# Kernel tuning notes

Hardware: AMD Instinct MI355X
Metric: run time of the kernel (lower is better)

Reference implementation:

```python
import jax, jax.numpy as jnp
import numpy as np

B, H, W, C = 16, 64, 64, 384
DH = 32                 # dim_head
NH = C // DH            # heads = dim // dim_head
WS = 8                  # window_size
DFF = 4 * C             # dim_ff default = 4*dim
EPS = 1e-5


def setup_inputs() -> dict:
    key = jax.random.key(0)
    ks = jax.random.split(key, 6)
    rn = lambda k, shape, scale: (jax.random.normal(k, shape, jnp.float32) * scale)
    return {
        "x": rn(ks[0], (B, H, W, C), 1.0),
        "w_qkv": rn(ks[1], (C, 3 * NH * DH), 0.02),   # fused qkv projection, bias=False
        "w_out": rn(ks[2], (NH * DH, C), 0.02),       # attention output projection
        "gamma_attn": jnp.ones((C,), jnp.float32),     # LayerNormNoBias2d weight (post-attn)
        "w1": rn(ks[3], (C, DFF), 0.02),               # FFN up projection
        "w2": rn(ks[4], (DFF, C), 0.02),               # FFN down projection
        "gamma_ff": jnp.ones((C,), jnp.float32),       # LayerNormNoBias2d weight (post-FFN)
    }


def _shift2d(x):
    # S2-MLP style 4-way spatial shift of channel quarters, zero-filled at borders.
    c4 = x.shape[-1] // 4
    g1 = jnp.pad(x[:, :-1, :, 0 * c4:1 * c4], ((0, 0), (1, 0), (0, 0), (0, 0)))  # shift down
    g2 = jnp.pad(x[:, 1:, :, 1 * c4:2 * c4], ((0, 0), (0, 1), (0, 0), (0, 0)))   # shift up
    g3 = jnp.pad(x[:, :, :-1, 2 * c4:3 * c4], ((0, 0), (0, 0), (1, 0), (0, 0)))  # shift right
    g4 = jnp.pad(x[:, :, 1:, 3 * c4:4 * c4], ((0, 0), (0, 0), (0, 1), (0, 0)))   # shift left
    return jnp.concatenate([g1, g2, g3, g4], axis=-1)


def _ln_nobias(x, gamma):
    # LayerNorm over channel dim, weight only (no bias).
    mu = jnp.mean(x, axis=-1, keepdims=True)
    var = jnp.var(x, axis=-1, keepdims=True)
    return (x - mu) * jax.lax.rsqrt(var + EPS) * gamma


def _window_attention(x, w_qkv, w_out):
    # Grouped (non-overlapping) window multi-head self-attention.
    b, h, w, c = x.shape
    nh, nw = h // WS, w // WS
    T = WS * WS
    # partition into windows: (b*nh*nw, T, c)
    xw = x.reshape(b, nh, WS, nw, WS, c).transpose(0, 1, 3, 2, 4, 5).reshape(b * nh * nw, T, c)
    qkv = xw @ w_qkv                                   # (n, T, 3*NH*DH)
    qkv = qkv.reshape(-1, T, 3, NH, DH)
    q = qkv[:, :, 0].transpose(0, 2, 1, 3)             # (n, NH, T, DH)
    k = qkv[:, :, 1].transpose(0, 2, 1, 3)
    v = qkv[:, :, 2].transpose(0, 2, 1, 3)
    logits = jnp.einsum('nhqd,nhkd->nhqk', q, k) * (DH ** -0.5)
    attn = jax.nn.softmax(logits, axis=-1)
    o = jnp.einsum('nhqk,nhkd->nhqd', attn, v)         # (n, NH, T, DH)
    o = o.transpose(0, 2, 1, 3).reshape(-1, T, NH * DH) @ w_out
    # un-window back to (b, h, w, c)
    return o.reshape(b, nh, nw, WS, WS, c).transpose(0, 1, 3, 2, 4, 5).reshape(b, h, w, c)


def reference(x, w_qkv, w_out, gamma_attn, w1, w2, gamma_ff):
    # x = x + DropBlock(Norm(GWAttn(Shift2d(x))))   (drop rates = 0 -> identity)
    a = _window_attention(_shift2d(x), w_qkv, w_out)
    x = x + _ln_nobias(a, gamma_attn)
    # x = x + DropBlock(Norm(FF(x)))
    f = jax.nn.gelu(x @ w1, approximate=False) @ w2
    return x + _ln_nobias(f, gamma_ff)
```

## Files before the change

kernel.cpp:

```cpp
#include <hip/hip_runtime.h>
#include <hip/hip_bf16.h>
#include <math.h>

typedef __attribute__((ext_vector_type(8))) __bf16 bf16x8;
typedef __attribute__((ext_vector_type(4))) float f32x4;
typedef unsigned int uint32;

static constexpr int kC   = 384;
static constexpr int kNH  = 12;
static constexpr int kDH  = 32;
static constexpr int kT   = 64;
static constexpr int kH   = 64;
static constexpr int kW   = 64;
static constexpr int kDFF = 1536;
static constexpr long kNTOK = 65536;
static constexpr long kNT  = kNTOK * kC;

__device__ __forceinline__ float bf_lo(uint32 u){ return __uint_as_float(u << 16); }
__device__ __forceinline__ float bf_hi(uint32 u){ return __uint_as_float(u & 0xffff0000u); }

__device__ __forceinline__ float gelu_fast(float x) {
    float x2 = x * x;
    float t  = fmaf(0.102944787f, x2, 2.302208165f);
    float m  = fminf(x * t, 80.0f);
    float e  = __builtin_amdgcn_exp2f(m);
    float d  = 1.0f + e;
    return x * e * __builtin_amdgcn_rcpf(d);
}

__global__ void k_transpose_cast(const float* __restrict__ src, __bf16* __restrict__ dst,
                                 int K, int N)
{
    int o = blockIdx.x * 256 + threadIdx.x;
    if (o >= K * N) return;
    int n = o / K, k = o - n * K;
    dst[o] = (__bf16)src[(size_t)k * N + n];
}

__global__ __launch_bounds__(256) void k_shift_window(const float* __restrict__ x,
                                                      __bf16* __restrict__ Aw)
{
    int tid = blockIdx.x * 256 + threadIdx.x;
    int m = tid / 48;
    int g = tid - m * 48;
    int c0 = g * 8;
    int wi = m >> 6, t = m & 63;
    int b = wi >> 6, nh = (wi >> 3) & 7, nw = wi & 7;
    int h = nh * 8 + (t >> 3);
    int w = nw * 8 + (t & 7);
    int q = c0 / 96;
    int sh = h, sw = w;
    bool ok;
    if      (q == 0) { sh = h - 1; ok = (h >= 1);  }
    else if (q == 1) { sh = h + 1; ok = (h <= 62); }
    else if (q == 2) { sw = w - 1; ok = (w >= 1);  }
    else             { sw = w + 1; ok = (w <= 62); }

    __bf16 r[8] __attribute__((aligned(16)));
    if (ok) {
        const float4* src = reinterpret_cast<const float4*>(
            x + (((size_t)b * kH + sh) * kW + sw) * kC + c0);
        float4 v0 = src[0], v1 = src[1];
        r[0] = (__bf16)v0.x; r[1] = (__bf16)v0.y; r[2] = (__bf16)v0.z; r[3] = (__bf16)v0.w;
        r[4] = (__bf16)v1.x; r[5] = (__bf16)v1.y; r[6] = (__bf16)v1.z; r[7] = (__bf16)v1.w;
    } else {
        #pragma unroll
        for (int i = 0; i < 8; ++i) r[i] = (__bf16)0.0f;
    }
    *reinterpret_cast<int4*>(Aw + (size_t)m * kC + c0) = *reinterpret_cast<int4*>(r);
}

template<int EPI>
__global__ __launch_bounds__(512) void k_gemm(const __bf16* __restrict__ A,
                                              const __bf16* __restrict__ B,
                                              __bf16* __restrict__ Cout,
                                              int N, int K, int nt)
{
    __shared__ __align__(16) __bf16 As[2][256 * 32];
    __shared__ __align__(16) __bf16 Bs[2][128 * 32];
    const int tid  = threadIdx.x;
    const int wave = tid >> 6, lane = tid & 63;
    const int g = lane >> 4, qh = lane & 15;

    const int nwg = gridDim.x;
    const int wg  = (blockIdx.x & 7) * (nwg >> 3) + (blockIdx.x >> 3);
    const int nb  = wg % nt, mb = wg / nt;
    const int m0 = mb * 256, n0 = nb * 128;
    const int wr = (wave >> 1) * 64;
    const int wc = (wave & 1) * 64;

    const int sw = ((g ^ ((lane >> 1) & 3)) << 3);

    auto STAGE = [&](int buf, int t) {
        const int k0 = t << 5;
        #pragma unroll
        for (int i = 0; i < 2; ++i) {
            int idx = tid + i * 512;
            int row = idx >> 2;
            int gseg = (idx & 3) ^ ((idx >> 3) & 3);
            __builtin_amdgcn_global_load_lds(
                (const __attribute__((address_space(1))) void*)(A + (size_t)(m0 + row) * K + k0 + gseg * 8),
                (__attribute__((address_space(3))) void*)(&As[buf][idx * 8]), 16, 0, 0);
        }
        {
            int idx = tid;
            int row = idx >> 2;
            int gseg = (idx & 3) ^ ((idx >> 3) & 3);
            __builtin_amdgcn_global_load_lds(
                (const __attribute__((address_space(1))) void*)(B + (size_t)(n0 + row) * K + k0 + gseg * 8),
                (__attribute__((address_space(3))) void*)(&Bs[buf][idx * 8]), 16, 0, 0);
        }
    };

    f32x4 acc[4][4] = {};
    const int nkt = K >> 5;

    STAGE(0, 0);
    for (int t = 0; t < nkt; ++t) {
        const int cur = t & 1;
        __syncthreads();
        if (t + 1 < nkt) STAGE(cur ^ 1, t + 1);

        bf16x8 af[4], bfr[4];
        #pragma unroll
        for (int mi = 0; mi < 4; ++mi) {
            int ra = wr + mi * 16 + qh;
            af[mi] = *reinterpret_cast<const bf16x8*>(&As[cur][ra * 32 + sw]);
        }
        #pragma unroll
        for (int ni = 0; ni < 4; ++ni) {
            int rb = wc + ni * 16 + qh;
            bfr[ni] = *reinterpret_cast<const bf16x8*>(&Bs[cur][rb * 32 + sw]);
        }
        __builtin_amdgcn_s_setprio(1);
        #pragma unroll
        for (int mi = 0; mi < 4; ++mi)
            #pragma unroll
            for (int ni = 0; ni < 4; ++ni)
                acc[mi][ni] = __builtin_amdgcn_mfma_f32_16x16x32_bf16(af[mi], bfr[ni], acc[mi][ni], 0, 0, 0);
        __builtin_amdgcn_s_setprio(0);
    }

    #pragma unroll
    for (int ni = 0; ni < 4; ++ni) {
        const int col = n0 + wc + ni * 16 + qh;
        size_t cbase = 0;
        if constexpr (EPI == 0) {
            int s   = col / 384;
            int rem = col - s * 384;
            int hh  = rem >> 5, d = rem & 31;
            cbase = (size_t)s * kNT + ((size_t)hh * 64) * kDH + d;
        }
        #pragma unroll
        for (int mi = 0; mi < 4; ++mi) {
            #pragma unroll
            for (int r = 0; r < 4; ++r) {
                int row = m0 + wr + mi * 16 + (g << 2) + r;
                float v = acc[mi][ni][r];
                if constexpr (EPI == 0) {
                    Cout[cbase + ((size_t)(row >> 6) * kNH * 64 + (row & 63)) * kDH] = (__bf16)v;
                } else if constexpr (EPI == 1) {
                    Cout[(size_t)row * N + col] = (__bf16)v;
                } else {
                    Cout[(size_t)row * N + col] = (__bf16)gelu_fast(v);
                }
            }
        }
    }
}

__global__ __launch_bounds__(256) void k_attn(const __bf16* __restrict__ qkv,
                                              __bf16* __restrict__ AO)
{
    __shared__ __bf16 Pl[4][kT * kT];
    const int wave = threadIdx.x >> 6, lane = threadIdx.x & 63;
    const int pair = blockIdx.x * 4 + wave;
    const int wi = pair / kNH, hh = pair - wi * kNH;
    const int g = lane >> 4, qh = lane & 15;

    const __bf16* Qp = qkv + ((size_t)wi * kNH + hh) * (kT * kDH);
    const __bf16* Kp = Qp + kNT;
    const __bf16* Vp = Qp + 2 * kNT;
    char* Pb = (char*)&Pl[wave][0];

    bf16x8 qa[4], kb[4];
    #pragma unroll
    for (int mi = 0; mi < 4; ++mi)
        qa[mi] = *reinterpret_cast<const bf16x8*>(Qp + (mi * 16 + qh) * kDH + g * 8);
    #pragma unroll
    for (int ni = 0; ni < 4; ++ni)
        kb[ni] = *reinterpret_cast<const bf16x8*>(Kp + (ni * 16 + qh) * kDH + g * 8);

    f32x4 s[4][4] = {};
    #pragma unroll
    for (int mi = 0; mi < 4; ++mi)
        #pragma unroll
        for (int ni = 0; ni < 4; ++ni)
            s[mi][ni] = __builtin_amdgcn_mfma_f32_16x16x32_bf16(qa[mi], kb[ni], s[mi][ni], 0, 0, 0);

    const float scale = 0.17677669529663687f;
    float rmax[4][4], rsum[4][4];
    #pragma unroll
    for (int mi = 0; mi < 4; ++mi)
        #pragma unroll
        for (int r = 0; r < 4; ++r) {
            float a = fmaxf(fmaxf(s[mi][0][r], s[mi][1][r]), fmaxf(s[mi][2][r], s[mi][3][r]));
            #pragma unroll
            for (int st = 1; st < 16; st <<= 1) a = fmaxf(a, __shfl_xor(a, st));
            rmax[mi][r] = a;
        }
    #pragma unroll
    for (int mi = 0; mi < 4; ++mi)
        #pragma unroll
        for (int r = 0; r < 4; ++r) {
            float acc = 0.f;
            #pragma unroll
            for (int ni = 0; ni < 4; ++ni) {
                float p = __expf((s[mi][ni][r] - rmax[mi][r]) * scale);
                s[mi][ni][r] = p;
                acc += p;
            }
            #pragma unroll
            for (int st = 1; st < 16; st <<= 1) acc += __shfl_xor(acc, st);
            rsum[mi][r] = 1.0f / acc;
        }

    #pragma unroll
    for (int mi = 0; mi < 4; ++mi)
        #pragma unroll
        for (int ni = 0; ni < 4; ++ni)
            #pragma unroll
            for (int r = 0; r < 4; ++r) {
                int row = mi * 16 + g * 4 + r;
                int col = ni * 16 + qh;
                uint32 byte = (uint32)((row << 7) | (col << 1)) ^ (uint32)((row & 7) << 4);
                *reinterpret_cast<__bf16*>(Pb + byte) = (__bf16)s[mi][ni][r];
            }

    f32x4 o[4][2] = {};
    #pragma unroll
    for (int kk = 0; kk < 2; ++kk) {
        bf16x8 pa[4], vb[2];
        #pragma unroll
        for (int mi = 0; mi < 4; ++mi) {
            int row = mi * 16 + qh;
            uint32 byte = (uint32)((row << 7) | (kk << 6) | (g << 4)) ^ (uint32)((row & 7) << 4);
            pa[mi] = *reinterpret_cast<const bf16x8*>(Pb + byte);
        }
        #pragma unroll
        for (int n2 = 0; n2 < 2; ++n2) {
            __bf16 tmp[8];
            #pragma unroll
            for (int j = 0; j < 8; ++j)
                tmp[j] = Vp[(kk * 32 + g * 8 + j) * kDH + n2 * 16 + qh];
            vb[n2] = *reinterpret_cast<const bf16x8*>(tmp);
        }
        #pragma unroll
        for (int mi = 0; mi < 4; ++mi)
            #pragma unroll
            for (int n2 = 0; n2 < 2; ++n2)
                o[mi][n2] = __builtin_amdgcn_mfma_f32_16x16x32_bf16(pa[mi], vb[n2], o[mi][n2], 0, 0, 0);
    }

    #pragma unroll
    for (int mi = 0; mi < 4; ++mi)
        #pragma unroll
        for (int n2 = 0; n2 < 2; ++n2)
            #pragma unroll
            for (int r = 0; r < 4; ++r) {
                int row = mi * 16 + g * 4 + r;
                AO[((size_t)wi * 64 + row) * kC + hh * kDH + n2 * 16 + qh] =
                    (__bf16)(o[mi][n2][r] * rsum[mi][r]);
            }
}

__global__ __launch_bounds__(256) void k_ln_res1(const __bf16* __restrict__ P,
                                                 const float* __restrict__ x,
                                                 const float* __restrict__ gamma,
                                                 __bf16* __restrict__ X1)
{
    const int wave = threadIdx.x >> 6, lane = threadIdx.x & 63;
    const int tok = blockIdx.x * 4 + wave;
    const int b = tok >> 12, hw = tok & 4095, h = hw >> 6, w = hw & 63;
    const int m = (((b << 6) | ((h >> 3) << 3) | (w >> 3)) << 6) | (((h & 7) << 3) | (w & 7));

    float p[6]; float sum = 0.f, sq = 0.f;
    #pragma unroll
    for (int i = 0; i < 6; ++i) {
        p[i] = (float)P[(size_t)m * kC + lane + i * 64];
        sum += p[i]; sq += p[i] * p[i];
    }
    #pragma unroll
    for (int off = 32; off; off >>= 1) { sum += __shfl_xor(sum, off); sq += __shfl_xor(sq, off); }
    float mean = sum * (1.0f / kC);
    float var  = sq * (1.0f / kC) - mean * mean;
    float rs   = rsqrtf(var + 1e-5f);
    #pragma unroll
    for (int i = 0; i < 6; ++i) {
        int c = lane + i * 64;
        float v = x[(size_t)tok * kC + c] + (p[i] - mean) * rs * gamma[c];
        X1[(size_t)tok * kC + c] = (__bf16)v;
    }
}

__global__ __launch_bounds__(256) void k_ln_res2(const __bf16* __restrict__ F,
                                                 const __bf16* __restrict__ X1,
                                                 const float* __restrict__ gamma,
                                                 float* __restrict__ out)
{
    const int wave = threadIdx.x >> 6, lane = threadIdx.x & 63;
    const size_t tok = blockIdx.x * 4 + wave;

    float f[6]; float sum = 0.f, sq = 0.f;
    #pragma unroll
    for (int i = 0; i < 6; ++i) {
        f[i] = (float)F[tok * kC + lane + i * 64];
        sum += f[i]; sq += f[i] * f[i];
    }
    #pragma unroll
    for (int off = 32; off; off >>= 1) { sum += __shfl_xor(sum, off); sq += __shfl_xor(sq, off); }
    float mean = sum * (1.0f / kC);
    float var  = sq * (1.0f / kC) - mean * mean;
    float rs   = rsqrtf(var + 1e-5f);
    #pragma unroll
    for (int i = 0; i < 6; ++i) {
        int c = lane + i * 64;
        out[tok * kC + c] = (float)X1[tok * kC + c] + (f[i] - mean) * rs * gamma[c];
    }
}

extern "C" void kernel_launch(void* const* d_in, const int* in_sizes, int n_in,
                              void* d_out, int out_size, void* d_ws, size_t ws_size,
                              hipStream_t stream) {
    const float* x    = (const float*)d_in[0];
    const float* wqkv = (const float*)d_in[1];
    const float* wout = (const float*)d_in[2];
    const float* g_at = (const float*)d_in[3];
    const float* w1   = (const float*)d_in[4];
    const float* w2   = (const float*)d_in[5];
    const float* g_ff = (const float*)d_in[6];
    float* out = (float*)d_out;

    char* ws = (char*)d_ws;
    size_t off = 0;
    auto alloc = [&](size_t bytes) { size_t o = off; off += (bytes + 255) & ~(size_t)255; return o; };
    __bf16* WqkvT = (__bf16*)(ws + alloc((size_t)1152 * 384 * 2));
    __bf16* WoutT = (__bf16*)(ws + alloc((size_t)384 * 384 * 2));
    __bf16* W1T   = (__bf16*)(ws + alloc((size_t)1536 * 384 * 2));
    __bf16* W2T   = (__bf16*)(ws + alloc((size_t)384 * 1536 * 2));
    __bf16* R1    = (__bf16*)(ws + alloc((size_t)kNTOK * kDFF * 2));
    __bf16* R2    = (__bf16*)(ws + alloc((size_t)kNT * 2));
    __bf16* R3    = (__bf16*)(ws + alloc((size_t)kNT * 2));

    k_transpose_cast<<<dim3((384 * 1152 + 255) / 256), 256, 0, stream>>>(wqkv, WqkvT, 384, 1152);
    k_transpose_cast<<<dim3((384 * 384 + 255) / 256), 256, 0, stream>>>(wout, WoutT, 384, 384);
    k_transpose_cast<<<dim3((384 * 1536 + 255) / 256), 256, 0, stream>>>(w1, W1T, 384, 1536);
    k_transpose_cast<<<dim3((1536 * 384 + 255) / 256), 256, 0, stream>>>(w2, W2T, 1536, 384);

    k_shift_window<<<dim3(12288), 256, 0, stream>>>(x, R2);

    k_gemm<0><<<dim3(256 * 9), 512, 0, stream>>>(R2, WqkvT, R1, 1152, 384, 9);

    k_attn<<<dim3(3072), 256, 0, stream>>>(R1, R2);

    k_gemm<1><<<dim3(256 * 3), 512, 0, stream>>>(R2, WoutT, R3, 384, 384, 3);

    k_ln_res1<<<dim3(16384), 256, 0, stream>>>(R3, x, g_at, R2);

    k_gemm<2><<<dim3(256 * 12), 512, 0, stream>>>(R2, W1T, R1, 1536, 384, 12);

    k_gemm<1><<<dim3(256 * 3), 512, 0, stream>>>(R1, W2T, R3, 384, 1536, 3);

    k_ln_res2<<<dim3(16384), 256, 0, stream>>>(R3, R2, g_ff, out);
}
```

Baseline: 510.9 us.

## Triple-buffer A tiles in GEMM with explicit vmcnt waits and deeper prefetch

New measurement: 509.8 us. No clear change (-0.2%).

```diff
diff --git a/kernel.cpp b/kernel.cpp
--- a/kernel.cpp
+++ b/kernel.cpp
@@ -76,7 +76,7 @@
                                               __bf16* __restrict__ Cout,
                                               int N, int K, int nt)
 {
-    __shared__ __align__(16) __bf16 As[2][256 * 32];
+    __shared__ __align__(16) __bf16 As[3][256 * 32];
     __shared__ __align__(16) __bf16 Bs[2][128 * 32];
     const int tid  = threadIdx.x;
     const int wave = tid >> 6, lane = tid & 63;
@@ -91,7 +91,7 @@
 
     const int sw = ((g ^ ((lane >> 1) & 3)) << 3);
 
-    auto STAGE = [&](int buf, int t) {
+    auto STAGE_A = [&](int buf, int t) {
         const int k0 = t << 5;
         #pragma unroll
         for (int i = 0; i < 2; ++i) {
@@ -102,35 +102,48 @@
                 (const __attribute__((address_space(1))) void*)(A + (size_t)(m0 + row) * K + k0 + gseg * 8),
                 (__attribute__((address_space(3))) void*)(&As[buf][idx * 8]), 16, 0, 0);
         }
-        {
-            int idx = tid;
-            int row = idx >> 2;
-            int gseg = (idx & 3) ^ ((idx >> 3) & 3);
-            __builtin_amdgcn_global_load_lds(
-                (const __attribute__((address_space(1))) void*)(B + (size_t)(n0 + row) * K + k0 + gseg * 8),
-                (__attribute__((address_space(3))) void*)(&Bs[buf][idx * 8]), 16, 0, 0);
-        }
+    };
+    auto STAGE_B = [&](int buf, int t) {
+        const int k0 = t << 5;
+        int idx = tid;
+        int row = idx >> 2;
+        int gseg = (idx & 3) ^ ((idx >> 3) & 3);
+        __builtin_amdgcn_global_load_lds(
+            (const __attribute__((address_space(1))) void*)(B + (size_t)(n0 + row) * K + k0 + gseg * 8),
+            (__attribute__((address_space(3))) void*)(&Bs[buf][idx * 8]), 16, 0, 0);
     };
 
     f32x4 acc[4][4] = {};
     const int nkt = K >> 5;
 
-    STAGE(0, 0);
+    STAGE_A(0, 0);
+    __builtin_amdgcn_sched_barrier(0);
+    STAGE_B(0, 0);
+    __builtin_amdgcn_sched_barrier(0);
+    STAGE_A(1, 1);
+    __builtin_amdgcn_sched_barrier(0);
+
+    int ca = 0, sa = 2;
     for (int t = 0; t < nkt; ++t) {
-        const int cur = t & 1;
-        __syncthreads();
-        if (t + 1 < nkt) STAGE(cur ^ 1, t + 1);
+        if (t + 1 < nkt) asm volatile("s_waitcnt vmcnt(2)" ::: "memory");
+        else             asm volatile("s_waitcnt vmcnt(0)" ::: "memory");
+        __builtin_amdgcn_s_barrier();
+        __builtin_amdgcn_sched_barrier(0);
+        if (t + 1 < nkt) STAGE_B((t + 1) & 1, t + 1);
+        __builtin_amdgcn_sched_barrier(0);
+        if (t + 2 < nkt) STAGE_A(sa, t + 2);
+        __builtin_amdgcn_sched_barrier(0);
 
         bf16x8 af[4], bfr[4];
         #pragma unroll
         for (int mi = 0; mi < 4; ++mi) {
             int ra = wr + mi * 16 + qh;
-            af[mi] = *reinterpret_cast<const bf16x8*>(&As[cur][ra * 32 + sw]);
+            af[mi] = *reinterpret_cast<const bf16x8*>(&As[ca][ra * 32 + sw]);
         }
         #pragma unroll
         for (int ni = 0; ni < 4; ++ni) {
             int rb = wc + ni * 16 + qh;
-            bfr[ni] = *reinterpret_cast<const bf16x8*>(&Bs[cur][rb * 32 + sw]);
+            bfr[ni] = *reinterpret_cast<const bf16x8*>(&Bs[t & 1][rb * 32 + sw]);
         }
         __builtin_amdgcn_s_setprio(1);
         #pragma unroll
@@ -139,6 +152,9 @@
             for (int ni = 0; ni < 4; ++ni)
                 acc[mi][ni] = __builtin_amdgcn_mfma_f32_16x16x32_bf16(af[mi], bfr[ni], acc[mi][ni], 0, 0, 0);
         __builtin_amdgcn_s_setprio(0);
+
+        ca = (ca == 2) ? 0 : ca + 1;
+        sa = (sa == 2) ? 0 : sa + 1;
     }
 
     #pragma unroll
```
